# Performance work log

Hardware: AMD Instinct MI355X
Metric: run time of the kernel (lower is better)

## Reference

```python
import jax, jax.numpy as jnp
import numpy as np

B, T, C = 8, 4096, 128


def setup_inputs() -> dict:
    key = jax.random.key(0)
    ks = jax.random.split(key, 9)
    s = 0.05
    return {
        "inputs": jax.random.normal(ks[0], (B, T, C), dtype=jnp.float32),
        "Wq": jax.random.normal(ks[1], (C, C), dtype=jnp.float32) * s,
        "bq": jnp.zeros((C,), dtype=jnp.float32),
        "Wk": jax.random.normal(ks[2], (C, C), dtype=jnp.float32) * s,
        "bk": jnp.zeros((C,), dtype=jnp.float32),
        "Wv": jax.random.normal(ks[3], (C, C), dtype=jnp.float32) * s,
        "bv": jnp.zeros((C,), dtype=jnp.float32),
        "Wa": jax.random.normal(ks[4], (C, C), dtype=jnp.float32) * s,
        "ba": jnp.zeros((C,), dtype=jnp.float32),
        "alpha": jnp.full((1,), 0.5, dtype=jnp.float32),
    }


def reference(inputs, Wq, bq, Wk, bk, Wv, bv, Wa, ba, alpha):
    # 1x1 Conv1D == per-timestep dense projection: [B,T,C] @ [C,F] + b
    q = jnp.einsum("btc,cf->btf", inputs, Wq) + bq
    k = jnp.einsum("btc,cf->btf", inputs, Wk) + bk
    v = jnp.einsum("btc,cf->btf", inputs, Wv) + bv
    # full attention, no scaling (matches source)
    scores = jnp.einsum("btf,bsf->bts", q, k)  # [B,T,T]
    attn = jax.nn.softmax(scores, axis=-1)
    attn_out = jnp.einsum("bts,bsf->btf", attn, v)
    feat = jnp.einsum("btf,fg->btg", attn_out, Wa) + ba
    return feat * alpha * inputs
```

## Files before the change

kernel.cpp:

```cpp
#include <hip/hip_runtime.h>


typedef short short8 __attribute__((ext_vector_type(8)));
typedef float f32x4 __attribute__((ext_vector_type(4)));

constexpr int BB = 8;
constexpr int TT = 4096;
constexpr int CC = 128;

__device__ inline unsigned int f2bf(float f) {
  union { float f; unsigned int u; } c; c.f = f;
  unsigned int u = c.u;
  u += 0x7fffu + ((u >> 16) & 1u);
  return u >> 16;
}

__global__ __launch_bounds__(256) void wprep_kernel(
    const float* __restrict__ Wq, const float* __restrict__ Wk,
    const float* __restrict__ Wv, const float* __restrict__ Wa,
    unsigned short* __restrict__ Wt)
{
  __shared__ unsigned short ld[128 * 136];
  const int t = threadIdx.x;
  const int m = blockIdx.x;
  const float* W = (m == 0) ? Wq : (m == 1) ? Wk : (m == 2) ? Wv : Wa;
  unsigned short* o = Wt + (size_t)m * CC * CC;
#pragma unroll
  for (int i = 0; i < 16; ++i) {
    int chunk = t + 256 * i;
    int c = chunk >> 5, f4 = (chunk & 31) * 4;
    float4 v = *(const float4*)(W + (size_t)c * CC + f4);
    uint2 u;
    u.x = f2bf(v.x) | (f2bf(v.y) << 16);
    u.y = f2bf(v.z) | (f2bf(v.w) << 16);
    *(uint2*)(ld + c * 136 + f4) = u;
  }
  __syncthreads();
#pragma unroll
  for (int i = 0; i < 16; ++i) {
    int chunk = t + 256 * i;
    int f = chunk >> 5, c4 = (chunk & 31) * 4;
    unsigned int a0 = ld[(c4 + 0) * 136 + f];
    unsigned int a1 = ld[(c4 + 1) * 136 + f];
    unsigned int a2 = ld[(c4 + 2) * 136 + f];
    unsigned int a3 = ld[(c4 + 3) * 136 + f];
    uint2 u;
    u.x = a0 | (a1 << 16);
    u.y = a2 | (a3 << 16);
    *(uint2*)(o + f * CC + c4) = u;
  }
}

__global__ __launch_bounds__(256) void qkv_kernel(
    const float* __restrict__ x, const unsigned short* __restrict__ Wt,
    const float* __restrict__ bq, const float* __restrict__ bk,
    const float* __restrict__ bv,
    unsigned short* __restrict__ Qo, unsigned short* __restrict__ Ko,
    unsigned short* __restrict__ Vo)
{
  __shared__ unsigned short xs[128 * 128];
  __shared__ unsigned short wt[128 * 128];
  const int t = threadIdx.x;
  const int tile = blockIdx.x;

#pragma unroll
  for (int i = 0; i < 16; ++i) {
    int chunk = t + 256 * i;
    int row = chunk >> 5, c4 = chunk & 31;
    float4 v = *(const float4*)(x + (size_t)(tile * 128 + row) * CC + c4 * 4);
    uint2 u;
    u.x = f2bf(v.x) | (f2bf(v.y) << 16);
    u.y = f2bf(v.z) | (f2bf(v.w) << 16);
    unsigned int byte = (unsigned)(row * 256 + c4 * 8) ^ (((unsigned)row & 7) << 4);
    *(uint2*)((char*)xs + byte) = u;
  }

  const int w = t >> 6, l = t & 63, lr = l & 15, lh = l >> 4;

#pragma unroll
  for (int m = 0; m < 3; ++m) {
    __syncthreads();
#pragma unroll
    for (int i = 0; i < 8; ++i) {
      int chunk = t + 256 * i;
      int f = chunk >> 4, c16 = chunk & 15;
      uint4 d = *(const uint4*)(Wt + (size_t)m * CC * CC + (size_t)f * CC + c16 * 8);
      unsigned int byte = (unsigned)(f * 256 + c16 * 16) ^ (((unsigned)f & 7) << 4);
      *(uint4*)((char*)wt + byte) = d;
    }
    __syncthreads();

    const float* bias = (m == 0) ? bq : (m == 1) ? bk : bv;
    unsigned short* out = (m == 0) ? Qo : (m == 1) ? Ko : Vo;

    f32x4 acc[2][8];
#pragma unroll
    for (int a = 0; a < 2; ++a)
#pragma unroll
      for (int n = 0; n < 8; ++n) acc[a][n] = (f32x4){0.f, 0.f, 0.f, 0.f};

#pragma unroll
    for (int kk = 0; kk < 4; ++kk) {
      short8 a[2];
#pragma unroll
      for (int rb = 0; rb < 2; ++rb) {
        int row = w * 32 + rb * 16 + lr;
        unsigned int byte = (unsigned)(row * 256 + kk * 64 + lh * 16) ^ (((unsigned)row & 7) << 4);
        a[rb] = *(const short8*)((const char*)xs + byte);
      }
#pragma unroll
      for (int n = 0; n < 8; ++n) {
        int row = n * 16 + lr;
        unsigned int byte = (unsigned)(row * 256 + kk * 64 + lh * 16) ^ (((unsigned)row & 7) << 4);
        short8 bfr = *(const short8*)((const char*)wt + byte);
        acc[0][n] = __builtin_amdgcn_mfma_f32_16x16x32_bf16(a[0], bfr, acc[0][n], 0, 0, 0);
        acc[1][n] = __builtin_amdgcn_mfma_f32_16x16x32_bf16(a[1], bfr, acc[1][n], 0, 0, 0);
      }
    }
#pragma unroll
    for (int n = 0; n < 8; ++n) {
      int col = n * 16 + lr;
      float bc = bias[col];
#pragma unroll
      for (int rb = 0; rb < 2; ++rb)
#pragma unroll
        for (int r = 0; r < 4; ++r) {
          int row = tile * 128 + w * 32 + rb * 16 + lh * 4 + r;
          out[(size_t)row * CC + col] = (unsigned short)f2bf(acc[rb][n][r] + bc);
        }
    }
  }
}

__global__ __launch_bounds__(256) void vtrans_kernel(
    const unsigned short* __restrict__ V, unsigned short* __restrict__ Vt)
{
  __shared__ unsigned short tile[64 * 136];
  const int t = threadIdx.x;
  const int b = blockIdx.y;
  const int kv0 = blockIdx.x * 64;
  const unsigned short* Vb = V + (size_t)b * TT * CC;
  unsigned short* Vtb = Vt + (size_t)b * TT * CC;
#pragma unroll
  for (int i = 0; i < 4; ++i) {
    int chunk = t + 256 * i;
    int row = chunk >> 4, c16 = chunk & 15;
    uint4 d = *(const uint4*)(Vb + (size_t)(kv0 + row) * CC + c16 * 8);
    *(uint4*)(tile + row * 136 + c16 * 8) = d;
  }
  __syncthreads();
#pragma unroll
  for (int i = 0; i < 4; ++i) {
    int chunk = t + 256 * i;
    int dd = chunk >> 3, kc = chunk & 7;
    unsigned short tmp[8];
#pragma unroll
    for (int j = 0; j < 8; ++j) tmp[j] = tile[(kc * 8 + j) * 136 + dd];
    uint4 u;
    u.x = (unsigned)tmp[0] | ((unsigned)tmp[1] << 16);
    u.y = (unsigned)tmp[2] | ((unsigned)tmp[3] << 16);
    u.z = (unsigned)tmp[4] | ((unsigned)tmp[5] << 16);
    u.w = (unsigned)tmp[6] | ((unsigned)tmp[7] << 16);
    *(uint4*)(Vtb + (size_t)dd * TT + kv0 + kc * 8) = u;
  }
}

__global__ __launch_bounds__(256, 2) void flash_kernel(
    const unsigned short* __restrict__ Q,
    const unsigned short* __restrict__ K,
    const unsigned short* __restrict__ Vt,
    unsigned short* __restrict__ AO)
{
  __shared__ unsigned short kt[64 * 128];
  __shared__ unsigned short vt[128 * 64];
  __shared__ unsigned short ps[4][16 * 64];
  const int t = threadIdx.x, w = t >> 6, l = t & 63, lr = l & 15, lh = l >> 4;
  const int bid = blockIdx.x;
  const int b = bid & 7;
  const int q0 = (bid >> 3) * 64;
  const unsigned short* Qb  = Q  + (size_t)b * TT * CC;
  const unsigned short* Kb  = K  + (size_t)b * TT * CC;
  const unsigned short* Vtb = Vt + (size_t)b * TT * CC;

  short8 qf[4];
  {
    int qrow = q0 + w * 16 + lr;
#pragma unroll
    for (int kk = 0; kk < 4; ++kk)
      qf[kk] = *(const short8*)(Qb + (size_t)qrow * CC + kk * 32 + lh * 8);
  }

  const int c0 = t, c1 = t + 256, c2 = t + 512, c3 = t + 768;
  const int kr0 = c0 >> 4, kr1 = c1 >> 4, kr2 = c2 >> 4, kr3 = c3 >> 4;
  const int kb0 = (c0 & 15) * 16, kb1 = (c1 & 15) * 16,
            kb2 = (c2 & 15) * 16, kb3 = (c3 & 15) * 16;
  const unsigned int kd0 = ((unsigned)(kr0 * 256 + kb0)) ^ (((unsigned)kr0 & 7) << 4);
  const unsigned int kd1 = ((unsigned)(kr1 * 256 + kb1)) ^ (((unsigned)kr1 & 7) << 4);
  const unsigned int kd2 = ((unsigned)(kr2 * 256 + kb2)) ^ (((unsigned)kr2 & 7) << 4);
  const unsigned int kd3 = ((unsigned)(kr3 * 256 + kb3)) ^ (((unsigned)kr3 & 7) << 4);
  const int dr0 = c0 >> 3, dr1 = c1 >> 3, dr2 = c2 >> 3, dr3 = c3 >> 3;
  const int vb0 = (c0 & 7) * 16, vb1 = (c1 & 7) * 16,
            vb2 = (c2 & 7) * 16, vb3 = (c3 & 7) * 16;
  const unsigned int vd0 = ((unsigned)(dr0 * 128 + vb0)) ^ (((unsigned)dr0 & 7) << 4);
  const unsigned int vd1 = ((unsigned)(dr1 * 128 + vb1)) ^ (((unsigned)dr1 & 7) << 4);
  const unsigned int vd2 = ((unsigned)(dr2 * 128 + vb2)) ^ (((unsigned)dr2 & 7) << 4);
  const unsigned int vd3 = ((unsigned)(dr3 * 128 + vb3)) ^ (((unsigned)dr3 & 7) << 4);

  f32x4 ao[8];
#pragma unroll
  for (int n = 0; n < 8; ++n) ao[n] = (f32x4){0.f, 0.f, 0.f, 0.f};
  float llp = 0.f;

  uint4 k0 = *(const uint4*)(Kb + (size_t)kr0 * CC + (kb0 >> 1));
  uint4 k1 = *(const uint4*)(Kb + (size_t)kr1 * CC + (kb1 >> 1));
  uint4 k2 = *(const uint4*)(Kb + (size_t)kr2 * CC + (kb2 >> 1));
  uint4 k3 = *(const uint4*)(Kb + (size_t)kr3 * CC + (kb3 >> 1));
  uint4 v0 = *(const uint4*)(Vtb + (size_t)dr0 * TT + (vb0 >> 1));
  uint4 v1 = *(const uint4*)(Vtb + (size_t)dr1 * TT + (vb1 >> 1));
  uint4 v2 = *(const uint4*)(Vtb + (size_t)dr2 * TT + (vb2 >> 1));
  uint4 v3 = *(const uint4*)(Vtb + (size_t)dr3 * TT + (vb3 >> 1));

  constexpr int NT = TT / 64;
  for (int tile = 0; tile < NT; ++tile) {
    __syncthreads();
    *(uint4*)((char*)kt + kd0) = k0;
    *(uint4*)((char*)kt + kd1) = k1;
    *(uint4*)((char*)kt + kd2) = k2;
    *(uint4*)((char*)kt + kd3) = k3;
    *(uint4*)((char*)vt + vd0) = v0;
    *(uint4*)((char*)vt + vd1) = v1;
    *(uint4*)((char*)vt + vd2) = v2;
    *(uint4*)((char*)vt + vd3) = v3;
    __syncthreads();
    if (tile + 1 < NT) {
      int kv0 = (tile + 1) * 64;
      k0 = *(const uint4*)(Kb + (size_t)(kv0 + kr0) * CC + (kb0 >> 1));
      k1 = *(const uint4*)(Kb + (size_t)(kv0 + kr1) * CC + (kb1 >> 1));
      k2 = *(const uint4*)(Kb + (size_t)(kv0 + kr2) * CC + (kb2 >> 1));
      k3 = *(const uint4*)(Kb + (size_t)(kv0 + kr3) * CC + (kb3 >> 1));
      v0 = *(const uint4*)(Vtb + (size_t)dr0 * TT + kv0 + (vb0 >> 1));
      v1 = *(const uint4*)(Vtb + (size_t)dr1 * TT + kv0 + (vb1 >> 1));
      v2 = *(const uint4*)(Vtb + (size_t)dr2 * TT + kv0 + (vb2 >> 1));
      v3 = *(const uint4*)(Vtb + (size_t)dr3 * TT + kv0 + (vb3 >> 1));
    }

    f32x4 s[4];
#pragma unroll
    for (int n = 0; n < 4; ++n) s[n] = (f32x4){0.f, 0.f, 0.f, 0.f};
#pragma unroll
    for (int n = 0; n < 4; ++n) {
#pragma unroll
      for (int kk = 0; kk < 4; ++kk) {
        int row = n * 16 + lr;
        unsigned int byte = ((unsigned)(row * 256 + kk * 64 + lh * 16)) ^ (((unsigned)row & 7) << 4);
        short8 kfr = *(const short8*)((const char*)kt + byte);
        s[n] = __builtin_amdgcn_mfma_f32_16x16x32_bf16(kfr, qf[kk], s[n], 0, 0, 0);
      }
    }

    unsigned int pswz = ((unsigned)lr & 7) << 4;
#pragma unroll
    for (int n = 0; n < 4; ++n) {
      float p0 = __expf(s[n][0]);
      float p1 = __expf(s[n][1]);
      float p2 = __expf(s[n][2]);
      float p3 = __expf(s[n][3]);
      llp += (p0 + p1) + (p2 + p3);
      uint2 u;
      u.x = f2bf(p0) | (f2bf(p1) << 16);
      u.y = f2bf(p2) | (f2bf(p3) << 16);
      unsigned int byte = ((unsigned)(lr * 128 + n * 32 + lh * 8)) ^ pswz;
      *(uint2*)((char*)(&ps[w][0]) + byte) = u;
    }

    short8 pf[2];
#pragma unroll
    for (int kk2 = 0; kk2 < 2; ++kk2) {
      unsigned int byte = ((unsigned)(lr * 128 + kk2 * 64 + lh * 16)) ^ pswz;
      pf[kk2] = *(const short8*)((const char*)(&ps[w][0]) + byte);
    }
#pragma unroll
    for (int n = 0; n < 8; ++n) {
#pragma unroll
      for (int kk2 = 0; kk2 < 2; ++kk2) {
        int row = n * 16 + lr;
        unsigned int byte = ((unsigned)(row * 128 + kk2 * 64 + lh * 16)) ^ (((unsigned)row & 7) << 4);
        short8 vfr = *(const short8*)((const char*)vt + byte);
        ao[n] = __builtin_amdgcn_mfma_f32_16x16x32_bf16(pf[kk2], vfr, ao[n], 0, 0, 0);
      }
    }
  }

  unsigned short* AOb = AO + (size_t)b * TT * CC;
  float s1 = llp + __shfl_xor(llp, 16, 64);
  float s2 = s1 + __shfl_xor(s1, 32, 64);
  float inv = 1.0f / s2;
  float ivr[4];
#pragma unroll
  for (int r = 0; r < 4; ++r) ivr[r] = __shfl(inv, lh * 4 + r, 64);
#pragma unroll
  for (int n = 0; n < 8; ++n)
#pragma unroll
    for (int r = 0; r < 4; ++r) {
      int row = q0 + w * 16 + lh * 4 + r;
      int col = n * 16 + lr;
      AOb[(size_t)row * CC + col] = (unsigned short)f2bf(ao[n][r] * ivr[r]);
    }
}

__global__ __launch_bounds__(256) void outproj_kernel(
    const unsigned short* __restrict__ AO, const unsigned short* __restrict__ Wta,
    const float* __restrict__ ba, const float* __restrict__ x,
    const float* __restrict__ alpha, float* __restrict__ out)
{
  __shared__ unsigned short as_[128 * 128];
  __shared__ unsigned short wt[128 * 128];
  const int t = threadIdx.x;
  const int tile = blockIdx.x;

#pragma unroll
  for (int i = 0; i < 8; ++i) {
    int chunk = t + 256 * i;
    int row = chunk >> 4, c16 = chunk & 15;
    uint4 d = *(const uint4*)(AO + (size_t)(tile * 128 + row) * CC + c16 * 8);
    unsigned int byte = (unsigned)(row * 256 + c16 * 16) ^ (((unsigned)row & 7) << 4);
    *(uint4*)((char*)as_ + byte) = d;
  }
#pragma unroll
  for (int i = 0; i < 8; ++i) {
    int chunk = t + 256 * i;
    int f = chunk >> 4, c16 = chunk & 15;
    uint4 d = *(const uint4*)(Wta + (size_t)f * CC + c16 * 8);
    unsigned int byte = (unsigned)(f * 256 + c16 * 16) ^ (((unsigned)f & 7) << 4);
    *(uint4*)((char*)wt + byte) = d;
  }
  __syncthreads();

  const int w = t >> 6, l = t & 63, lr = l & 15, lh = l >> 4;
  f32x4 acc[2][8];
#pragma unroll
  for (int a = 0; a < 2; ++a)
#pragma unroll
    for (int n = 0; n < 8; ++n) acc[a][n] = (f32x4){0.f, 0.f, 0.f, 0.f};

#pragma unroll
  for (int kk = 0; kk < 4; ++kk) {
    short8 a[2];
#pragma unroll
    for (int rb = 0; rb < 2; ++rb) {
      int row = w * 32 + rb * 16 + lr;
      unsigned int byte = (unsigned)(row * 256 + kk * 64 + lh * 16) ^ (((unsigned)row & 7) << 4);
      a[rb] = *(const short8*)((const char*)as_ + byte);
    }
#pragma unroll
    for (int n = 0; n < 8; ++n) {
      int row = n * 16 + lr;
      unsigned int byte = (unsigned)(row * 256 + kk * 64 + lh * 16) ^ (((unsigned)row & 7) << 4);
      short8 bfr = *(const short8*)((const char*)wt + byte);
      acc[0][n] = __builtin_amdgcn_mfma_f32_16x16x32_bf16(a[0], bfr, acc[0][n], 0, 0, 0);
      acc[1][n] = __builtin_amdgcn_mfma_f32_16x16x32_bf16(a[1], bfr, acc[1][n], 0, 0, 0);
    }
  }

  const float a0 = alpha[0];
#pragma unroll
  for (int n = 0; n < 8; ++n) {
    int col = n * 16 + lr;
    float bc = ba[col];
#pragma unroll
    for (int rb = 0; rb < 2; ++rb)
#pragma unroll
      for (int r = 0; r < 4; ++r) {
        int row = tile * 128 + w * 32 + rb * 16 + lh * 4 + r;
        size_t idx = (size_t)row * CC + col;
        out[idx] = (acc[rb][n][r] + bc) * a0 * x[idx];
      }
  }
}

extern "C" void kernel_launch(void* const* d_in, const int* in_sizes, int n_in,
                              void* d_out, int out_size, void* d_ws, size_t ws_size,
                              hipStream_t stream) {
  const float* x     = (const float*)d_in[0];
  const float* Wq    = (const float*)d_in[1];
  const float* bq    = (const float*)d_in[2];
  const float* Wk    = (const float*)d_in[3];
  const float* bk    = (const float*)d_in[4];
  const float* Wv    = (const float*)d_in[5];
  const float* bv    = (const float*)d_in[6];
  const float* Wa    = (const float*)d_in[7];
  const float* ba    = (const float*)d_in[8];
  const float* alpha = (const float*)d_in[9];
  float* out = (float*)d_out;

  char* ws = (char*)d_ws;
  const size_t MAT = (size_t)BB * TT * CC * sizeof(unsigned short);
  unsigned short* Q  = (unsigned short*)(ws);
  unsigned short* K  = (unsigned short*)(ws + MAT);
  unsigned short* V  = (unsigned short*)(ws + 2 * MAT);
  unsigned short* Vt = (unsigned short*)(ws + 3 * MAT);
  unsigned short* AO = (unsigned short*)(ws + 2 * MAT);
  unsigned short* Wt = (unsigned short*)(ws + 4 * MAT);

  wprep_kernel<<<dim3(4), 256, 0, stream>>>(Wq, Wk, Wv, Wa, Wt);
  qkv_kernel<<<dim3(256), 256, 0, stream>>>(x, Wt, bq, bk, bv, Q, K, V);
  vtrans_kernel<<<dim3(64, 8), 256, 0, stream>>>(V, Vt);
  flash_kernel<<<dim3(512), 256, 0, stream>>>(Q, K, Vt, AO);
  outproj_kernel<<<dim3(256), 256, 0, stream>>>(AO, Wt + 3 * (size_t)CC * CC, ba, x, alpha, out);
}
```

Measured before the change: 216.4 us.

## Double-buffer K/V tiles in shared memory to halve barriers per iteration

Splits the K and V LDS tiles into two buffers. The next tile is written into the alternate buffer mid-iteration, after the softmax, and a single barrier closes each iteration instead of two. The goal is to drop one barrier per tile and overlap the LDS stores with compute. LDS use grows from about 40KB to about 72KB per block, which may limit the two-blocks-per-CU occupancy target.

```diff
diff --git a/kernel.cpp b/kernel.cpp
--- a/kernel.cpp
+++ b/kernel.cpp
@@ -171,8 +171,8 @@
     const unsigned short* __restrict__ Vt,
     unsigned short* __restrict__ AO)
 {
-  __shared__ unsigned short kt[64 * 128];
-  __shared__ unsigned short vt[128 * 64];
+  __shared__ unsigned short kt[2][64 * 128];
+  __shared__ unsigned short vt[2][128 * 64];
   __shared__ unsigned short ps[4][16 * 64];
   const int t = threadIdx.x, w = t >> 6, l = t & 63, lr = l & 15, lh = l >> 4;
   const int bid = blockIdx.x;
@@ -220,19 +220,21 @@
   uint4 v2 = *(const uint4*)(Vtb + (size_t)dr2 * TT + (vb2 >> 1));
   uint4 v3 = *(const uint4*)(Vtb + (size_t)dr3 * TT + (vb3 >> 1));
 
+  {
+    char* ktp = (char*)(&kt[0][0]);
+    char* vtp = (char*)(&vt[0][0]);
+    *(uint4*)(ktp + kd0) = k0; *(uint4*)(ktp + kd1) = k1;
+    *(uint4*)(ktp + kd2) = k2; *(uint4*)(ktp + kd3) = k3;
+    *(uint4*)(vtp + vd0) = v0; *(uint4*)(vtp + vd1) = v1;
+    *(uint4*)(vtp + vd2) = v2; *(uint4*)(vtp + vd3) = v3;
+  }
+  __syncthreads();
+
   constexpr int NT = TT / 64;
+  int p = 0;
   for (int tile = 0; tile < NT; ++tile) {
-    __syncthreads();
-    *(uint4*)((char*)kt + kd0) = k0;
-    *(uint4*)((char*)kt + kd1) = k1;
-    *(uint4*)((char*)kt + kd2) = k2;
-    *(uint4*)((char*)kt + kd3) = k3;
-    *(uint4*)((char*)vt + vd0) = v0;
-    *(uint4*)((char*)vt + vd1) = v1;
-    *(uint4*)((char*)vt + vd2) = v2;
-    *(uint4*)((char*)vt + vd3) = v3;
-    __syncthreads();
-    if (tile + 1 < NT) {
+    const bool more = (tile + 1 < NT);
+    if (more) {
       int kv0 = (tile + 1) * 64;
       k0 = *(const uint4*)(Kb + (size_t)(kv0 + kr0) * CC + (kb0 >> 1));
       k1 = *(const uint4*)(Kb + (size_t)(kv0 + kr1) * CC + (kb1 >> 1));
@@ -244,6 +246,9 @@
       v3 = *(const uint4*)(Vtb + (size_t)dr3 * TT + kv0 + (vb3 >> 1));
     }
 
+    const char* kb_ = (const char*)(&kt[p][0]);
+    const char* vb_ = (const char*)(&vt[p][0]);
+
     f32x4 s[4];
 #pragma unroll
     for (int n = 0; n < 4; ++n) s[n] = (f32x4){0.f, 0.f, 0.f, 0.f};
@@ -253,7 +258,7 @@
       for (int kk = 0; kk < 4; ++kk) {
         int row = n * 16 + lr;
         unsigned int byte = ((unsigned)(row * 256 + kk * 64 + lh * 16)) ^ (((unsigned)row & 7) << 4);
-        short8 kfr = *(const short8*)((const char*)kt + byte);
+        short8 kfr = *(const short8*)(kb_ + byte);
         s[n] = __builtin_amdgcn_mfma_f32_16x16x32_bf16(kfr, qf[kk], s[n], 0, 0, 0);
       }
     }
@@ -273,6 +278,15 @@
       *(uint2*)((char*)(&ps[w][0]) + byte) = u;
     }
 
+    if (more) {
+      char* ktn = (char*)(&kt[p ^ 1][0]);
+      char* vtn = (char*)(&vt[p ^ 1][0]);
+      *(uint4*)(ktn + kd0) = k0; *(uint4*)(ktn + kd1) = k1;
+      *(uint4*)(ktn + kd2) = k2; *(uint4*)(ktn + kd3) = k3;
+      *(uint4*)(vtn + vd0) = v0; *(uint4*)(vtn + vd1) = v1;
+      *(uint4*)(vtn + vd2) = v2; *(uint4*)(vtn + vd3) = v3;
+    }
+
     short8 pf[2];
 #pragma unroll
     for (int kk2 = 0; kk2 < 2; ++kk2) {
@@ -285,10 +299,13 @@
       for (int kk2 = 0; kk2 < 2; ++kk2) {
         int row = n * 16 + lr;
         unsigned int byte = ((unsigned)(row * 128 + kk2 * 64 + lh * 16)) ^ (((unsigned)row & 7) << 4);
-        short8 vfr = *(const short8*)((const char*)vt + byte);
+        short8 vfr = *(const short8*)(vb_ + byte);
         ao[n] = __builtin_amdgcn_mfma_f32_16x16x32_bf16(pf[kk2], vfr, ao[n], 0, 0, 0);
       }
     }
+
+    __syncthreads();
+    p ^= 1;
   }
 
   unsigned short* AOb = AO + (size_t)b * TT * CC;
```

Result: slower. 221.2 us (+2.2%).
